# Optimization experiments

Hardware: AMD Instinct MI355X
Metric: run time of the kernel (lower is better)

The kernel has to match this reference:

```python
import jax, jax.numpy as jnp
import numpy as np

N = 100000   # batched tree nodes
WD = 300     # word_dim
TD = 50      # tag_dim
M = 168      # mem_dim


def setup_inputs() -> dict:
    key = jax.random.key(0)
    ks = jax.random.split(key, 17)
    rn = lambda k, shp: jax.random.normal(k, shp, dtype=jnp.float32)
    w = lambda k, shp: jax.random.normal(k, shp, dtype=jnp.float32) * 0.05
    return {
        "e": rn(ks[0], (N, WD)),
        "tag": rn(ks[1], (N, TD)),
        "tag_parent": rn(ks[2], (N, TD)),
        "h_prev": rn(ks[3], (N, M)),
        "c_prev": rn(ks[4], (N, M)),
        "k": rn(ks[5], (N, M)),
        "q": rn(ks[6], (N, M)),
        # Leaf cell: 4 gates (i, o, f_left, u), each with We/Wt/Wtp/Uh linears,
        # fused as stacked [in_dim, 4*M] matrices + one fused bias.
        "We_l": w(ks[7], (WD, 4 * M)),
        "Wt_l": w(ks[8], (TD, 4 * M)),
        "Wtp_l": w(ks[9], (TD, 4 * M)),
        "Uh_l": w(ks[10], (M, 4 * M)),
        "b_l": w(ks[11], (4 * M,)),
        # Node cell: 5 gates (i, o, f_left, f_down, u) with Wt/Wtp/Uh; the Uk
        # (child-sum k) linear is only applied to the first 4 gates (u omits it,
        # per the source).
        "Wt_n": w(ks[12], (TD, 5 * M)),
        "Wtp_n": w(ks[13], (TD, 5 * M)),
        "Uh_n": w(ks[14], (M, 5 * M)),
        "Uk_n": w(ks[15], (M, 4 * M)),
        "b_n": w(ks[16], (5 * M,)),
    }


def reference(e, tag, tag_parent, h_prev, c_prev, k, q,
              We_l, Wt_l, Wtp_l, Uh_l, b_l,
              Wt_n, Wtp_n, Uh_n, Uk_n, b_n):
    sig, tanh = jax.nn.sigmoid, jnp.tanh
    # ---- LeafModule ----
    pre = e @ We_l + tag @ Wt_l + tag_parent @ Wtp_l + h_prev @ Uh_l + b_l  # [N, 4M]
    i, o, fl, u = jnp.split(pre, 4, axis=-1)
    c1 = sig(i) * tanh(u) + sig(fl) * c_prev
    h1 = sig(o) * tanh(c1)
    # ---- NodeModule (consumes leaf state as h_prev / c_prev) ----
    pre5 = tag @ Wt_n + tag_parent @ Wtp_n + h1 @ Uh_n + b_n  # [N, 5M]
    pre4 = k @ Uk_n                                            # [N, 4M]
    i2, o2, fl2, fd2, u2 = jnp.split(pre5, 5, axis=-1)
    ki, ko, kfl, kfd = jnp.split(pre4, 4, axis=-1)
    i2, o2, fl2, fd2 = i2 + ki, o2 + ko, fl2 + kfl, fd2 + kfd
    c2 = sig(i2) * tanh(u2) + sig(fd2) * q + sig(fl2) * c1
    h2 = sig(o2) * tanh(c2)
    return jnp.concatenate([h2, c2], axis=-1)  # [N, 2M]
```

## Files before the change

kernel.cpp:

```cpp
#include <hip/hip_runtime.h>
#include <hip/hip_bf16.h>

#define NROWS 100000

typedef __attribute__((ext_vector_type(8))) short bf16x8;
typedef __attribute__((ext_vector_type(4))) float f32x4;
typedef float f32x4a8 __attribute__((ext_vector_type(4), aligned(8)));

__device__ __forceinline__ short f2b(float f) {
  __hip_bfloat16 h = __float2bfloat16(f);
  short s;
  __builtin_memcpy(&s, &h, sizeof(s));
  return s;
}

__device__ __forceinline__ float b2f(unsigned short u) {
  unsigned v = ((unsigned)u) << 16;
  float f;
  __builtin_memcpy(&f, &v, sizeof(f));
  return f;
}

__device__ __forceinline__ float sigf(float x) { return 1.f / (1.f + __expf(-x)); }
__device__ __forceinline__ float tanh_f(float x) { return 1.f - 2.f / (__expf(2.f * x) + 1.f); }

__device__ __forceinline__ void gload_lds16(const void* g, void* l) {
  __builtin_amdgcn_global_load_lds((const __attribute__((address_space(1))) unsigned int*)g,
                                   (__attribute__((address_space(3))) unsigned int*)l, 16, 0, 0);
}

__global__ void pack_weights(const float* __restrict__ We_l, const float* __restrict__ Wt_l,
                             const float* __restrict__ Wtp_l, const float* __restrict__ Uh_l,
                             const float* __restrict__ b_l,
                             const float* __restrict__ Wt_n, const float* __restrict__ Wtp_n,
                             const float* __restrict__ Uh_n, const float* __restrict__ Uk_n,
                             const float* __restrict__ b_n,
                             unsigned short* __restrict__ B1, unsigned short* __restrict__ B2) {
  const int NB1 = 18 * 3 * 16 * 512;
  const int NB2 = 14 * 3 * 24 * 512;
  int idx = blockIdx.x * blockDim.x + threadIdx.x;
  if (idx < NB1) {
    int b = idx & 7, lane = (idx >> 3) & 63, t = idx >> 9;
    int ct = t % 16, mb = (t / 16) % 3, kt = t / 48;
    int k = kt * 32 + ((lane >> 4) << 3) + b;
    int gate = ct >> 2, mtl = ct & 3;
    int m = mb * 64 + mtl * 16 + (lane & 15);
    float v = 0.f;
    if (m < 168) {
      int col = gate * 168 + m;
      if (k < 300)       v = We_l[k * 672 + col];
      else if (k < 350)  v = Wt_l[(k - 300) * 672 + col];
      else if (k < 400)  v = Wtp_l[(k - 350) * 672 + col];
      else if (k < 568)  v = Uh_l[(k - 400) * 672 + col];
      else if (k == 568) v = b_l[col];
    }
    B1[idx] = (unsigned short)f2b(v);
  } else if (idx < NB1 + NB2) {
    int j = idx - NB1;
    int b = j & 7, lane = (j >> 3) & 63, t = j >> 9;
    int ct = t % 24, mb = (t / 24) % 3, kt = t / 72;
    int k = kt * 32 + ((lane >> 4) << 3) + b;
    int gate = ct >> 2, mtl = ct & 3;
    int m = mb * 64 + mtl * 16 + (lane & 15);
    float v = 0.f;
    if (ct < 20 && m < 168) {
      int col = gate * 168 + m;
      if (k < 50)        v = Wt_n[k * 840 + col];
      else if (k < 100)  v = Wtp_n[(k - 50) * 840 + col];
      else if (k < 268)  v = (gate < 4) ? Uk_n[(k - 100) * 672 + gate * 168 + m] : 0.f;
      else if (k < 436)  v = Uh_n[(k - 268) * 840 + col];
      else if (k == 436) v = b_n[col];
    }
    B2[j] = (unsigned short)f2b(v);
  }
}

__device__ __forceinline__ float4 ld4a8(const float* __restrict__ p) {
  f32x4a8 v = *(const f32x4a8*)p;
  return make_float4(v[0], v[1], v[2], v[3]);
}

#define G1_NKT 18
#define G1_LOADS 2

__global__ __launch_bounds__(512, 4) void gemm1_kernel(
    const float* __restrict__ e, const float* __restrict__ tg, const float* __restrict__ tp,
    const float* __restrict__ hp, const float* __restrict__ cprev,
    const char* __restrict__ B1, unsigned short* __restrict__ c1buf,
    unsigned short* __restrict__ h1buf) {
  __shared__ char bb[2][16 * 1024];
  __shared__ char ab[2][4096];
  const int tid = threadIdx.x;
  const int wave = tid >> 6, ln = tid & 63;
  const int rw = wave >> 2, cw = wave & 3;
  const int rowblk = blockIdx.x / 3, mb = blockIdx.x % 3;
  const int rbase = rowblk * 64 + rw * 32;
  const int c = ln & 15, rg = ln >> 4;

  const int srowt = tid >> 3;
  const int sks = tid & 7;
  int srow = rowblk * 64 + srowt;
  if (srow >= NROWS) srow = NROWS - 1;
  const int sphys = srowt * 64 + ((((sks >> 1) ^ ((srowt >> 1) & 3)) << 4)) + ((sks & 1) << 3);

  auto loadA = [&](int kt) -> float4 {
    const int c4 = kt * 32 + sks * 4;
    if (c4 + 4 <= 300) return *(const float4*)(e + srow * 300 + c4);
    if (c4 >= 300 && c4 + 4 <= 348) return ld4a8(tg + srow * 50 + (c4 - 300));
    if (c4 == 348)
      return make_float4(tg[srow * 50 + 48], tg[srow * 50 + 49], tp[srow * 50 + 0], tp[srow * 50 + 1]);
    if (c4 >= 352 && c4 + 4 <= 400) return ld4a8(tp + srow * 50 + (c4 - 350));
    if (c4 >= 400 && c4 + 4 <= 568) return *(const float4*)(hp + srow * 168 + (c4 - 400));
    if (c4 == 568) return make_float4(1.f, 0.f, 0.f, 0.f);
    return make_float4(0.f, 0.f, 0.f, 0.f);
  };
  auto storeA = [&](int buf, float4 v) {
    ushort4 w;
    w.x = (unsigned short)f2b(v.x); w.y = (unsigned short)f2b(v.y);
    w.z = (unsigned short)f2b(v.z); w.w = (unsigned short)f2b(v.w);
    *(ushort4*)&ab[buf][sphys] = w;
  };

  f32x4 acc[2][4];
  const f32x4 z4 = {0.f, 0.f, 0.f, 0.f};
#pragma unroll
  for (int a = 0; a < 2; ++a)
#pragma unroll
    for (int t = 0; t < 4; ++t) acc[a][t] = z4;

  storeA(0, loadA(0));
  const char* Bbase = B1 + (size_t)mb * 16384;
#pragma unroll
  for (int j = 0; j < G1_LOADS; ++j)
    gload_lds16(Bbase + (j * 512 + tid) * 16, &bb[0][(j * 512 + (wave << 6)) * 16]);
  float4 av = loadA(1);
  __syncthreads();

  const int r0t = rw * 32 + c, r1t = rw * 32 + 16 + c;
  const int aoff0 = r0t * 64 + ((rg ^ ((r0t >> 1) & 3)) << 4);
  const int aoff1 = r1t * 64 + ((rg ^ ((r1t >> 1) & 3)) << 4);

#pragma unroll
  for (int kt = 0; kt < G1_NKT; ++kt) {
    const int cur = kt & 1, nxt = cur ^ 1;
    bf16x8 a0 = *(const bf16x8*)&ab[cur][aoff0];
    bf16x8 a1 = *(const bf16x8*)&ab[cur][aoff1];
    bf16x8 bfr[4];
#pragma unroll
    for (int g = 0; g < 4; ++g)
      bfr[g] = *(const bf16x8*)&bb[cur][((((g << 2) + cw) << 6) + ln) * 16];
    if (kt + 1 < G1_NKT) {
      storeA(nxt, av);
      if (kt + 2 < G1_NKT) av = loadA(kt + 2);
      const char* g = B1 + ((size_t)(kt + 1) * 3 + mb) * 16384;
#pragma unroll
      for (int j = 0; j < G1_LOADS; ++j)
        gload_lds16(g + (j * 512 + tid) * 16, &bb[nxt][(j * 512 + (wave << 6)) * 16]);
    }
#pragma unroll
    for (int g = 0; g < 4; ++g) {
      acc[0][g] = __builtin_amdgcn_mfma_f32_16x16x32_bf16(a0, bfr[g], acc[0][g], 0, 0, 0);
      acc[1][g] = __builtin_amdgcn_mfma_f32_16x16x32_bf16(a1, bfr[g], acc[1][g], 0, 0, 0);
    }
    __syncthreads();
  }

  const int m = mb * 64 + cw * 16 + c;
  if (m < 168) {
#pragma unroll
    for (int rt = 0; rt < 2; ++rt) {
#pragma unroll
      for (int reg = 0; reg < 4; ++reg) {
        const int row = rbase + rt * 16 + (rg << 2) + reg;
        if (row >= NROWS) continue;
        const float iv = acc[rt][0][reg];
        const float ov = acc[rt][1][reg];
        const float fv = acc[rt][2][reg];
        const float uv = acc[rt][3][reg];
        const int off = row * 168 + m;
        const float cp = cprev[off];
        const float c1 = sigf(iv) * tanh_f(uv) + sigf(fv) * cp;
        const float h1 = sigf(ov) * tanh_f(c1);
        c1buf[off] = (unsigned short)f2b(c1);
        h1buf[off] = (unsigned short)f2b(h1);
      }
    }
  }
}

#define G2_NKT 14
#define G2_LOADS 3

__global__ __launch_bounds__(512, 4) void gemm2_kernel(
    const float* __restrict__ tg, const float* __restrict__ tp, const float* __restrict__ kk,
    const float* __restrict__ q, const char* __restrict__ B2,
    const unsigned short* __restrict__ c1buf, const unsigned short* __restrict__ h1buf,
    float* __restrict__ out) {
  __shared__ char bb[2][24 * 1024];
  __shared__ char ab[2][4096];
  const int tid = threadIdx.x;
  const int wave = tid >> 6, ln = tid & 63;
  const int rw = wave >> 2, cw = wave & 3;
  const int rowblk = blockIdx.x / 3, mb = blockIdx.x % 3;
  const int rbase = rowblk * 64 + rw * 32;
  const int c = ln & 15, rg = ln >> 4;

  const int srowt = tid >> 3;
  const int sks = tid & 7;
  int srow = rowblk * 64 + srowt;
  if (srow >= NROWS) srow = NROWS - 1;
  const int sphys = srowt * 64 + ((((sks >> 1) ^ ((srowt >> 1) & 3)) << 4)) + ((sks & 1) << 3);

  auto loadA = [&](int kt) -> float4 {
    const int c4 = kt * 32 + sks * 4;
    if (c4 + 4 <= 48) return ld4a8(tg + srow * 50 + c4);
    if (c4 == 48)
      return make_float4(tg[srow * 50 + 48], tg[srow * 50 + 49], tp[srow * 50 + 0], tp[srow * 50 + 1]);
    if (c4 >= 52 && c4 + 4 <= 100) return ld4a8(tp + srow * 50 + (c4 - 50));
    if (c4 >= 100 && c4 + 4 <= 268) return *(const float4*)(kk + srow * 168 + (c4 - 100));
    if (c4 >= 268 && c4 + 4 <= 436) {
      ushort4 w = *(const ushort4*)(h1buf + srow * 168 + (c4 - 268));
      return make_float4(b2f(w.x), b2f(w.y), b2f(w.z), b2f(w.w));
    }
    if (c4 == 436) return make_float4(1.f, 0.f, 0.f, 0.f);
    return make_float4(0.f, 0.f, 0.f, 0.f);
  };
  auto storeA = [&](int buf, float4 v) {
    ushort4 w;
    w.x = (unsigned short)f2b(v.x); w.y = (unsigned short)f2b(v.y);
    w.z = (unsigned short)f2b(v.z); w.w = (unsigned short)f2b(v.w);
    *(ushort4*)&ab[buf][sphys] = w;
  };

  f32x4 acc[2][5];
  const f32x4 z4 = {0.f, 0.f, 0.f, 0.f};
#pragma unroll
  for (int a = 0; a < 2; ++a)
#pragma unroll
    for (int t = 0; t < 5; ++t) acc[a][t] = z4;

  storeA(0, loadA(0));
  const char* Bbase = B2 + (size_t)mb * 24576;
#pragma unroll
  for (int j = 0; j < G2_LOADS; ++j)
    gload_lds16(Bbase + (j * 512 + tid) * 16, &bb[0][(j * 512 + (wave << 6)) * 16]);
  float4 av = loadA(1);
  __syncthreads();

  const int r0t = rw * 32 + c, r1t = rw * 32 + 16 + c;
  const int aoff0 = r0t * 64 + ((rg ^ ((r0t >> 1) & 3)) << 4);
  const int aoff1 = r1t * 64 + ((rg ^ ((r1t >> 1) & 3)) << 4);

#pragma unroll
  for (int kt = 0; kt < G2_NKT; ++kt) {
    const int cur = kt & 1, nxt = cur ^ 1;
    bf16x8 a0 = *(const bf16x8*)&ab[cur][aoff0];
    bf16x8 a1 = *(const bf16x8*)&ab[cur][aoff1];
    bf16x8 bfr[5];
#pragma unroll
    for (int g = 0; g < 5; ++g)
      bfr[g] = *(const bf16x8*)&bb[cur][((((g << 2) + cw) << 6) + ln) * 16];
    if (kt + 1 < G2_NKT) {
      storeA(nxt, av);
      if (kt + 2 < G2_NKT) av = loadA(kt + 2);
      const char* g = B2 + ((size_t)(kt + 1) * 3 + mb) * 24576;
#pragma unroll
      for (int j = 0; j < G2_LOADS; ++j)
        gload_lds16(g + (j * 512 + tid) * 16, &bb[nxt][(j * 512 + (wave << 6)) * 16]);
    }
#pragma unroll
    for (int g = 0; g < 5; ++g) {
      acc[0][g] = __builtin_amdgcn_mfma_f32_16x16x32_bf16(a0, bfr[g], acc[0][g], 0, 0, 0);
      acc[1][g] = __builtin_amdgcn_mfma_f32_16x16x32_bf16(a1, bfr[g], acc[1][g], 0, 0, 0);
    }
    __syncthreads();
  }

  const int m = mb * 64 + cw * 16 + c;
  if (m < 168) {
#pragma unroll
    for (int rt = 0; rt < 2; ++rt) {
#pragma unroll
      for (int reg = 0; reg < 4; ++reg) {
        const int row = rbase + rt * 16 + (rg << 2) + reg;
        if (row >= NROWS) continue;
        const float i2 = acc[rt][0][reg];
        const float o2 = acc[rt][1][reg];
        const float fl2 = acc[rt][2][reg];
        const float fd2 = acc[rt][3][reg];
        const float u2 = acc[rt][4][reg];
        const int off = row * 168 + m;
        const float c1 = b2f(c1buf[off]);
        const float qv = q[off];
        const float c2 = sigf(i2) * tanh_f(u2) + sigf(fd2) * qv + sigf(fl2) * c1;
        const float h2 = sigf(o2) * tanh_f(c2);
        out[row * 336 + m] = h2;
        out[row * 336 + 168 + m] = c2;
      }
    }
  }
}

extern "C" void kernel_launch(void* const* d_in, const int* in_sizes, int n_in,
                              void* d_out, int out_size, void* d_ws, size_t ws_size,
                              hipStream_t stream) {
  const float* e     = (const float*)d_in[0];
  const float* tag   = (const float*)d_in[1];
  const float* tagp  = (const float*)d_in[2];
  const float* hprev = (const float*)d_in[3];
  const float* cprev = (const float*)d_in[4];
  const float* kk    = (const float*)d_in[5];
  const float* q     = (const float*)d_in[6];
  const float* We_l  = (const float*)d_in[7];
  const float* Wt_l  = (const float*)d_in[8];
  const float* Wtp_l = (const float*)d_in[9];
  const float* Uh_l  = (const float*)d_in[10];
  const float* b_l   = (const float*)d_in[11];
  const float* Wt_n  = (const float*)d_in[12];
  const float* Wtp_n = (const float*)d_in[13];
  const float* Uh_n  = (const float*)d_in[14];
  const float* Uk_n  = (const float*)d_in[15];
  const float* b_n   = (const float*)d_in[16];
  float* out = (float*)d_out;

  char* ws = (char*)d_ws;
  unsigned short* B1 = (unsigned short*)ws;
  unsigned short* B2 = (unsigned short*)(ws + (1 << 20));
  unsigned short* c1buf = (unsigned short*)(ws + (3 << 20));
  unsigned short* h1buf = (unsigned short*)(ws + (3 << 20) + 33600000);

  const int NB = 18 * 3 * 16 * 512 + 14 * 3 * 24 * 512;
  pack_weights<<<(NB + 255) / 256, 256, 0, stream>>>(We_l, Wt_l, Wtp_l, Uh_l, b_l,
                                                     Wt_n, Wtp_n, Uh_n, Uk_n, b_n, B1, B2);

  const int nblk = ((NROWS + 63) / 64) * 3;
  gemm1_kernel<<<nblk, 512, 0, stream>>>(e, tag, tagp, hprev, cprev,
                                         (const char*)B1, c1buf, h1buf);
  gemm2_kernel<<<nblk, 512, 0, stream>>>(tag, tagp, kk, q,
                                         (const char*)B2, c1buf, h1buf, out);
}
```

Before: 489.7 us.

## Triple-buffer weight tiles with vmcnt waits and XCD-aware block mapping

Moves B-weight staging to a three-deep LDS ring so global-to-LDS loads for tile k+2 are in flight while tile k is computed. The full __syncthreads is replaced with explicit s_waitcnt vmcnt counts plus a raw barrier. Blocks are also remapped so the three column blocks of a row block share an XCD, which should improve L2 reuse of the A rows. This raises LDS per block, which may cut occupancy, and the hand-counted vmcnt values must match the number of outstanding loads for the results to stay correct.

```diff
diff --git a/kernel.cpp b/kernel.cpp
--- a/kernel.cpp
+++ b/kernel.cpp
@@ -2,6 +2,7 @@
 #include <hip/hip_bf16.h>
 
 #define NROWS 100000
+#define NRB 1563
 
 typedef __attribute__((ext_vector_type(8))) short bf16x8;
 typedef __attribute__((ext_vector_type(4))) float f32x4;
@@ -80,6 +81,13 @@
   return make_float4(v[0], v[1], v[2], v[3]);
 }
 
+__device__ __forceinline__ void xcd_decode(int bid, int& rowblk, int& mb) {
+  const int xcd = bid & 7;
+  const int j = bid >> 3;
+  rowblk = (j / 3) * 8 + xcd;
+  mb = j % 3;
+}
+
 #define G1_NKT 18
 #define G1_LOADS 2
 
@@ -88,12 +96,14 @@
     const float* __restrict__ hp, const float* __restrict__ cprev,
     const char* __restrict__ B1, unsigned short* __restrict__ c1buf,
     unsigned short* __restrict__ h1buf) {
-  __shared__ char bb[2][16 * 1024];
+  __shared__ char bb[3][16 * 1024];
   __shared__ char ab[2][4096];
+  int rowblk, mb;
+  xcd_decode(blockIdx.x, rowblk, mb);
+  if (rowblk >= NRB) return;
   const int tid = threadIdx.x;
   const int wave = tid >> 6, ln = tid & 63;
   const int rw = wave >> 2, cw = wave & 3;
-  const int rowblk = blockIdx.x / 3, mb = blockIdx.x % 3;
   const int rbase = rowblk * 64 + rw * 32;
   const int c = ln & 15, rg = ln >> 4;
 
@@ -120,6 +130,12 @@
     w.z = (unsigned short)f2b(v.z); w.w = (unsigned short)f2b(v.w);
     *(ushort4*)&ab[buf][sphys] = w;
   };
+  auto stageB = [&](int kt, int buf) {
+    const char* g = B1 + ((size_t)kt * 3 + mb) * 16384;
+#pragma unroll
+    for (int j = 0; j < G1_LOADS; ++j)
+      gload_lds16(g + (j * 512 + tid) * 16, &bb[buf][(j * 512 + (wave << 6)) * 16]);
+  };
 
   f32x4 acc[2][4];
   const f32x4 z4 = {0.f, 0.f, 0.f, 0.f};
@@ -129,12 +145,11 @@
     for (int t = 0; t < 4; ++t) acc[a][t] = z4;
 
   storeA(0, loadA(0));
-  const char* Bbase = B1 + (size_t)mb * 16384;
-#pragma unroll
-  for (int j = 0; j < G1_LOADS; ++j)
-    gload_lds16(Bbase + (j * 512 + tid) * 16, &bb[0][(j * 512 + (wave << 6)) * 16]);
+  stageB(0, 0);
   float4 av = loadA(1);
-  __syncthreads();
+  stageB(1, 1);
+  asm volatile("s_waitcnt vmcnt(3) lgkmcnt(0)" ::: "memory");
+  __builtin_amdgcn_s_barrier();
 
   const int r0t = rw * 32 + c, r1t = rw * 32 + 16 + c;
   const int aoff0 = r0t * 64 + ((rg ^ ((r0t >> 1) & 3)) << 4);
@@ -142,27 +157,32 @@
 
 #pragma unroll
   for (int kt = 0; kt < G1_NKT; ++kt) {
-    const int cur = kt & 1, nxt = cur ^ 1;
-    bf16x8 a0 = *(const bf16x8*)&ab[cur][aoff0];
-    bf16x8 a1 = *(const bf16x8*)&ab[cur][aoff1];
+    const int curB = kt % 3;
+    const int curA = kt & 1;
+    bf16x8 a0 = *(const bf16x8*)&ab[curA][aoff0];
+    bf16x8 a1 = *(const bf16x8*)&ab[curA][aoff1];
     bf16x8 bfr[4];
 #pragma unroll
     for (int g = 0; g < 4; ++g)
-      bfr[g] = *(const bf16x8*)&bb[cur][((((g << 2) + cw) << 6) + ln) * 16];
-    if (kt + 1 < G1_NKT) {
-      storeA(nxt, av);
-      if (kt + 2 < G1_NKT) av = loadA(kt + 2);
-      const char* g = B1 + ((size_t)(kt + 1) * 3 + mb) * 16384;
-#pragma unroll
-      for (int j = 0; j < G1_LOADS; ++j)
-        gload_lds16(g + (j * 512 + tid) * 16, &bb[nxt][(j * 512 + (wave << 6)) * 16]);
+      bfr[g] = *(const bf16x8*)&bb[curB][((((g << 2) + cw) << 6) + ln) * 16];
+    if (kt + 1 < G1_NKT) storeA(curA ^ 1, av);
+    if (kt + 2 < G1_NKT) {
+      av = loadA(kt + 2);
+      stageB(kt + 2, (kt + 2) % 3);
     }
 #pragma unroll
     for (int g = 0; g < 4; ++g) {
       acc[0][g] = __builtin_amdgcn_mfma_f32_16x16x32_bf16(a0, bfr[g], acc[0][g], 0, 0, 0);
       acc[1][g] = __builtin_amdgcn_mfma_f32_16x16x32_bf16(a1, bfr[g], acc[1][g], 0, 0, 0);
     }
-    __syncthreads();
+    if (kt + 1 < G1_NKT) {
+      if (kt + 2 < G1_NKT) {
+        asm volatile("s_waitcnt vmcnt(3) lgkmcnt(0)" ::: "memory");
+      } else {
+        asm volatile("s_waitcnt vmcnt(0) lgkmcnt(0)" ::: "memory");
+      }
+      __builtin_amdgcn_s_barrier();
+    }
   }
 
   const int m = mb * 64 + cw * 16 + c;
@@ -196,12 +216,14 @@
     const float* __restrict__ q, const char* __restrict__ B2,
     const unsigned short* __restrict__ c1buf, const unsigned short* __restrict__ h1buf,
     float* __restrict__ out) {
-  __shared__ char bb[2][24 * 1024];
+  __shared__ char bb[3][24 * 1024];
   __shared__ char ab[2][4096];
+  int rowblk, mb;
+  xcd_decode(blockIdx.x, rowblk, mb);
+  if (rowblk >= NRB) return;
   const int tid = threadIdx.x;
   const int wave = tid >> 6, ln = tid & 63;
   const int rw = wave >> 2, cw = wave & 3;
-  const int rowblk = blockIdx.x / 3, mb = blockIdx.x % 3;
   const int rbase = rowblk * 64 + rw * 32;
   const int c = ln & 15, rg = ln >> 4;
 
@@ -231,6 +253,12 @@
     w.z = (unsigned short)f2b(v.z); w.w = (unsigned short)f2b(v.w);
     *(ushort4*)&ab[buf][sphys] = w;
   };
+  auto stageB = [&](int kt, int buf) {
+    const char* g = B2 + ((size_t)kt * 3 + mb) * 24576;
+#pragma unroll
+    for (int j = 0; j < G2_LOADS; ++j)
+      gload_lds16(g + (j * 512 + tid) * 16, &bb[buf][(j * 512 + (wave << 6)) * 16]);
+  };
 
   f32x4 acc[2][5];
   const f32x4 z4 = {0.f, 0.f, 0.f, 0.f};
@@ -240,12 +268,11 @@
     for (int t = 0; t < 5; ++t) acc[a][t] = z4;
 
   storeA(0, loadA(0));
-  const char* Bbase = B2 + (size_t)mb * 24576;
-#pragma unroll
-  for (int j = 0; j < G2_LOADS; ++j)
-    gload_lds16(Bbase + (j * 512 + tid) * 16, &bb[0][(j * 512 + (wave << 6)) * 16]);
+  stageB(0, 0);
   float4 av = loadA(1);
-  __syncthreads();
+  stageB(1, 1);
+  asm volatile("s_waitcnt vmcnt(4) lgkmcnt(0)" ::: "memory");
+  __builtin_amdgcn_s_barrier();
 
   const int r0t = rw * 32 + c, r1t = rw * 32 + 16 + c;
   const int aoff0 = r0t * 64 + ((rg ^ ((r0t >> 1) & 3)) << 4);
@@ -253,27 +280,32 @@
 
 #pragma unroll
   for (int kt = 0; kt < G2_NKT; ++kt) {
-    const int cur = kt & 1, nxt = cur ^ 1;
-    bf16x8 a0 = *(const bf16x8*)&ab[cur][aoff0];
-    bf16x8 a1 = *(const bf16x8*)&ab[cur][aoff1];
+    const int curB = kt % 3;
+    const int curA = kt & 1;
+    bf16x8 a0 = *(const bf16x8*)&ab[curA][aoff0];
+    bf16x8 a1 = *(const bf16x8*)&ab[curA][aoff1];
     bf16x8 bfr[5];
 #pragma unroll
     for (int g = 0; g < 5; ++g)
-      bfr[g] = *(const bf16x8*)&bb[cur][((((g << 2) + cw) << 6) + ln) * 16];
-    if (kt + 1 < G2_NKT) {
-      storeA(nxt, av);
-      if (kt + 2 < G2_NKT) av = loadA(kt + 2);
-      const char* g = B2 + ((size_t)(kt + 1) * 3 + mb) * 24576;
-#pragma unroll
-      for (int j = 0; j < G2_LOADS; ++j)
-        gload_lds16(g + (j * 512 + tid) * 16, &bb[nxt][(j * 512 + (wave << 6)) * 16]);
+      bfr[g] = *(const bf16x8*)&bb[curB][((((g << 2) + cw) << 6) + ln) * 16];
+    if (kt + 1 < G2_NKT) storeA(curA ^ 1, av);
+    if (kt + 2 < G2_NKT) {
+      av = loadA(kt + 2);
+      stageB(kt + 2, (kt + 2) % 3);
     }
 #pragma unroll
     for (int g = 0; g < 5; ++g) {
       acc[0][g] = __builtin_amdgcn_mfma_f32_16x16x32_bf16(a0, bfr[g], acc[0][g], 0, 0, 0);
       acc[1][g] = __builtin_amdgcn_mfma_f32_16x16x32_bf16(a1, bfr[g], acc[1][g], 0, 0, 0);
     }
-    __syncthreads();
+    if (kt + 1 < G2_NKT) {
+      if (kt + 2 < G2_NKT) {
+        asm volatile("s_waitcnt vmcnt(4) lgkmcnt(0)" ::: "memory");
+      } else {
+        asm volatile("s_waitcnt vmcnt(0) lgkmcnt(0)" ::: "memory");
+      }
+      __builtin_amdgcn_s_barrier();
+    }
   }
 
   const int m = mb * 64 + cw * 16 + c;
@@ -333,7 +365,7 @@
   pack_weights<<<(NB + 255) / 256, 256, 0, stream>>>(We_l, Wt_l, Wtp_l, Uh_l, b_l,
                                                      Wt_n, Wtp_n, Uh_n, Uk_n, b_n, B1, B2);
 
-  const int nblk = ((NROWS + 63) / 64) * 3;
+  const int nblk = 4704;
   gemm1_kernel<<<nblk, 512, 0, stream>>>(e, tag, tagp, hprev, cprev,
                                          (const char*)B1, c1buf, h1buf);
   gemm2_kernel<<<nblk, 512, 0, stream>>>(tag, tagp, kk, q,
```

Result: faster. 428.3 us (-12.5%).
